# Optimization experiments

Hardware: AMD Instinct MI355X
Metric: run time of the kernel (lower is better)

Reference implementation:

```python
import jax, jax.numpy as jnp
import numpy as np

B, N, DIM = 2, 2048, 1024
NUM_HEADS = 16
EFF = NUM_HEADS // 2          # 8 effective heads
HD = DIM // NUM_HEADS         # 64
LAMBDA_INIT = 0.8
EPS = 1e-5


def setup_inputs() -> dict:
    key = jax.random.key(0)
    ks = jax.random.split(key, 16)
    s = 0.02
    return {
        "x":  jax.random.normal(ks[0], (B, N, DIM), dtype=jnp.float32),
        "Wq": jax.random.normal(ks[1], (DIM, DIM), dtype=jnp.float32) * s,
        "bq": jnp.zeros((DIM,), dtype=jnp.float32),
        "Wk": jax.random.normal(ks[2], (DIM, DIM), dtype=jnp.float32) * s,
        "bk": jnp.zeros((DIM,), dtype=jnp.float32),
        "Wv": jax.random.normal(ks[3], (DIM, DIM), dtype=jnp.float32) * s,
        "bv": jnp.zeros((DIM,), dtype=jnp.float32),
        "Wo": jax.random.normal(ks[4], (DIM, DIM), dtype=jnp.float32) * s,
        "bo": jnp.zeros((DIM,), dtype=jnp.float32),
        "norm_w": jnp.ones((2 * HD,), dtype=jnp.float32),
        "lq1": jax.random.normal(ks[5], (HD,), dtype=jnp.float32) * 0.1,
        "lk1": jax.random.normal(ks[6], (HD,), dtype=jnp.float32) * 0.1,
        "lq2": jax.random.normal(ks[7], (HD,), dtype=jnp.float32) * 0.1,
        "lk2": jax.random.normal(ks[8], (HD,), dtype=jnp.float32) * 0.1,
    }


def reference(x, Wq, bq, Wk, bk, Wv, bv, Wo, bo, norm_w, lq1, lk1, lq2, lk2):
    scale = HD ** -0.5
    # projections (torch Linear: y = x @ W.T + b)
    q = (x @ Wq.T + bq).reshape(B, N, NUM_HEADS, HD).transpose(0, 2, 1, 3) * scale  # [B,2E,N,hd]
    k = (x @ Wk.T + bk).reshape(B, N, NUM_HEADS, HD).transpose(0, 2, 1, 3)          # [B,2E,N,hd]
    v = (x @ Wv.T + bv).reshape(B, N, EFF, 2 * HD).transpose(0, 2, 1, 3)            # [B,E,N,2hd]

    scores = jnp.einsum('bhqd,bhkd->bhqk', q, k)              # [B,2E,N,N]
    probs = jax.nn.softmax(scores, axis=-1)
    probs = probs.reshape(B, EFF, 2, N, N)                    # pair consecutive heads

    lam = jnp.exp(jnp.sum(lq1 * lk1)) - jnp.exp(jnp.sum(lq2 * lk2)) + LAMBDA_INIT
    diff = probs[:, :, 0] - lam * probs[:, :, 1]              # [B,E,N,N]

    out = jnp.einsum('behk,bekd->behd'.replace('e','h').replace('hh','h') if False else 'bhqk,bhkd->bhqd', diff, v)  # [B,E,N,2hd]
    # headwise RMSNorm over last dim (2*hd)
    out = out * jax.lax.rsqrt(jnp.mean(out * out, axis=-1, keepdims=True) + EPS) * norm_w
    out = out * (1.0 - LAMBDA_INIT)

    out = out.transpose(0, 2, 1, 3).reshape(B, N, DIM)
    return out @ Wo.T + bo
```

## Files before the change

### kernel.cpp

```cpp
#include <hip/hip_runtime.h>
#include <hip/hip_bf16.h>

#define B_   2
#define N_   2048
#define DIM_ 1024
#define HD_  64
#define DV_  128

typedef __bf16 bf16;
typedef __bf16 bf16x8 __attribute__((ext_vector_type(8)));
typedef __bf16 bf16x4 __attribute__((ext_vector_type(4)));
typedef float  floatx4 __attribute__((ext_vector_type(4)));

#if __has_builtin(__builtin_amdgcn_exp2f)
#define EXP2(x) __builtin_amdgcn_exp2f(x)
#else
#define EXP2(x) exp2f(x)
#endif

#define QSCALE 0.1803368801111244f

__device__ __forceinline__ void async16(const void* g, void* l) {
  __builtin_amdgcn_global_load_lds(
      (__attribute__((address_space(1))) void*)g,
      (__attribute__((address_space(3))) void*)l, 16, 0, 0);
}

__global__ void convert_kernel(const float* __restrict__ x,
                               const float* __restrict__ wq,
                               const float* __restrict__ wk,
                               const float* __restrict__ wv,
                               const float* __restrict__ wo,
                               bf16* __restrict__ dst) {
  const int NX = B_ * N_ * DIM_;
  const int NW = DIM_ * DIM_;
  int i = (blockIdx.x * 256 + threadIdx.x) * 4;
  const float* src;
  int off;
  if (i < NX) { src = x; off = i; }
  else {
    int j = i - NX;
    int w = j >> 20;
    off = j & (NW - 1);
    src = (w == 0) ? wq : (w == 1) ? wk : (w == 2) ? wv : wo;
  }
  float4 v = *(const float4*)(src + off);
  bf16x4 o = { (bf16)v.x, (bf16)v.y, (bf16)v.z, (bf16)v.w };
  *(bf16x4*)(dst + i) = o;
}

__global__ void lam_kernel(const float* __restrict__ lq1, const float* __restrict__ lk1,
                           const float* __restrict__ lq2, const float* __restrict__ lk2,
                           float* __restrict__ lam_out) {
  int l = threadIdx.x;
  float a = lq1[l] * lk1[l];
  float b = lq2[l] * lk2[l];
  for (int m = 1; m < 64; m <<= 1) {
    a += __shfl_xor(a, m, 64);
    b += __shfl_xor(b, m, 64);
  }
  if (l == 0) *lam_out = __expf(a) - __expf(b) + 0.8f;
}

__global__ __launch_bounds__(256) void proj_kernel(
    const bf16* __restrict__ xb, const bf16* __restrict__ wall,
    const float* __restrict__ bq, const float* __restrict__ bk,
    const float* __restrict__ bv,
    bf16* __restrict__ qo, bf16* __restrict__ ko, bf16* __restrict__ vt) {
  __shared__ __align__(16) bf16 SM[2 * 128 * 64];
  bf16* At = SM;
  bf16* Bt = SM + 128 * 64;
  const int tid = threadIdx.x, lane = tid & 63, w = tid >> 6;
  const int tm = blockIdx.x, tn = blockIdx.y, z = blockIdx.z;
  const int quad = lane >> 4, l15 = lane & 15;
  const int wm = (w >> 1) * 64, wn = (w & 1) * 64;
  const bf16* Ab = xb + (long)tm * 128 * DIM_;
  const bf16* Bb = wall + (long)z * (DIM_ * DIM_) + (long)tn * 128 * DIM_;
  floatx4 zero = {0.f, 0.f, 0.f, 0.f};
  floatx4 acc[4][4];
#pragma unroll
  for (int i = 0; i < 4; ++i)
#pragma unroll
    for (int j = 0; j < 4; ++j) acc[i][j] = zero;

  for (int kb = 0; kb < DIM_ / 64; ++kb) {
    for (int idx = tid; idx < 1024; idx += 256) {
      int row = idx >> 3, ch = idx & 7, g = ch ^ (row & 7);
      async16(Ab + row * DIM_ + kb * 64 + g * 8, (char*)At + (idx - lane) * 16);
      async16(Bb + row * DIM_ + kb * 64 + g * 8, (char*)Bt + (idx - lane) * 16);
    }
    __syncthreads();
#pragma unroll
    for (int ks = 0; ks < 2; ++ks) {
      bf16x8 af[4], bfm[4];
#pragma unroll
      for (int mt = 0; mt < 4; ++mt) {
        int r = wm + mt * 16 + l15;
        af[mt] = *(const bf16x8*)&At[r * 64 + ((ks * 4 + quad) ^ (r & 7)) * 8];
      }
#pragma unroll
      for (int nt = 0; nt < 4; ++nt) {
        int r = wn + nt * 16 + l15;
        bfm[nt] = *(const bf16x8*)&Bt[r * 64 + ((ks * 4 + quad) ^ (r & 7)) * 8];
      }
#pragma unroll
      for (int mt = 0; mt < 4; ++mt)
#pragma unroll
        for (int nt = 0; nt < 4; ++nt)
          acc[mt][nt] = __builtin_amdgcn_mfma_f32_16x16x32_bf16(
              af[mt], bfm[nt], acc[mt][nt], 0, 0, 0);
    }
    __syncthreads();
  }

  if (z != 2) {
#pragma unroll
    for (int mt = 0; mt < 4; ++mt)
#pragma unroll
      for (int nt = 0; nt < 4; ++nt)
#pragma unroll
        for (int r = 0; r < 4; ++r) {
          int grow = tm * 128 + wm + mt * 16 + quad * 4 + r;
          int gcol = tn * 128 + wn + nt * 16 + l15;
          float v = acc[mt][nt][r];
          if (z == 0) {
            qo[(long)grow * DIM_ + gcol] = (bf16)((v + bq[gcol]) * QSCALE);
          } else {
            ko[(long)grow * DIM_ + gcol] = (bf16)(v + bk[gcol]);
          }
        }
  } else {
    bf16* Vl = SM;
#pragma unroll
    for (int nt = 0; nt < 4; ++nt) {
      int d = wn + nt * 16 + l15;
      float bvv = bv[tn * 128 + d];
      int m = (d & 7) * 2;
#pragma unroll
      for (int mt = 0; mt < 4; ++mt) {
        bf16x4 v4 = { (bf16)(acc[mt][nt][0] + bvv), (bf16)(acc[mt][nt][1] + bvv),
                      (bf16)(acc[mt][nt][2] + bvv), (bf16)(acc[mt][nt][3] + bvv) };
        int c = (wm >> 2) + mt * 4 + quad;
        *(bf16x4*)&Vl[d * 128 + (c ^ m) * 4] = v4;
      }
    }
    __syncthreads();
    const int bb = tm >> 4, e = tn;
    const long rowbase = ((long)(bb * 8 + e) * 128) * (long)N_ + (tm & 15) * 128;
#pragma unroll
    for (int p = 0; p < 8; ++p) {
      int d = p * 16 + (tid >> 4), j = tid & 15;
      int cs = (2 * j) ^ ((d & 7) * 2);
      bf16x8 val = *(const bf16x8*)&Vl[d * 128 + cs * 4];
      *(bf16x8*)&vt[rowbase + (long)d * N_ + j * 8] = val;
    }
  }
}

__global__ __launch_bounds__(256, 2) void attn_kernel(
    const bf16* __restrict__ qb, const bf16* __restrict__ kbuf,
    const bf16* __restrict__ vt, const float* __restrict__ lamp,
    const float* __restrict__ norm_w, bf16* __restrict__ ao) {
  __shared__ __align__(16) bf16 Kt[2][2 * 64 * 64];
  __shared__ __align__(16) bf16 Vt[2][128 * 64];
  __shared__ __align__(16) bf16 Pt[4][2][16 * 64];

  const int tid = threadIdx.x, lane = tid & 63, w = tid >> 6;
  const int qt = blockIdx.x, e = blockIdx.y, b = blockIdx.z;
  const int quad = lane >> 4, l15 = lane & 15;
  floatx4 zero = {0.f, 0.f, 0.f, 0.f};

  const int qrow = qt * 64 + w * 16 + l15;
  const bf16* qrp = qb + (long)(b * N_ + qrow) * DIM_ + e * 128;
  bf16x8 qf0[2], qf1[2];
  qf0[0] = *(const bf16x8*)(qrp + quad * 8);
  qf0[1] = *(const bf16x8*)(qrp + 32 + quad * 8);
  qf1[0] = *(const bf16x8*)(qrp + 64 + quad * 8);
  qf1[1] = *(const bf16x8*)(qrp + 96 + quad * 8);

  const bf16* kbase = kbuf + (long)b * N_ * DIM_ + e * 128;
  const bf16* vbase = vt + (long)(b * 8 + e) * DV_ * N_;

  floatx4 acc0[8], acc1[8];
#pragma unroll
  for (int i = 0; i < 8; ++i) { acc0[i] = zero; acc1[i] = zero; }
  float lp0 = 0.f, lp1 = 0.f;

  bf16* Pt0 = Pt[w][0];
  bf16* Pt1 = Pt[w][1];

#define STAGE(ktv, bufv)                                                            \
  {                                                                                 \
    int kt_ = (ktv), buf_ = (bufv);                                                 \
    _Pragma("unroll") for (int t = 0; t < 4; ++t) {                                 \
      int idx = tid + t * 256;                                                      \
      int khl = idx >> 9, row = (idx >> 3) & 63, ch = idx & 7, g = ch ^ (row & 7);  \
      async16(kbase + ((long)(kt_ * 64 + row)) * DIM_ + khl * 64 + g * 8,           \
              (char*)Kt[buf_] + (idx - lane) * 16);                                 \
    }                                                                               \
    _Pragma("unroll") for (int t = 0; t < 4; ++t) {                                 \
      int idx = tid + t * 256;                                                      \
      int row = idx >> 3, ch = idx & 7, g = ch ^ (row & 7);                         \
      async16(vbase + (long)row * N_ + kt_ * 64 + g * 8,                            \
              (char*)Vt[buf_] + (idx - lane) * 16);                                 \
    }                                                                               \
  }

  STAGE(0, 0);

  for (int kt = 0; kt < N_ / 64; ++kt) {
    const int buf = kt & 1;
    __syncthreads();
    if (kt + 1 < N_ / 64) STAGE(kt + 1, buf ^ 1);

    const bf16* Kh0 = Kt[buf];
    const bf16* Kh1 = Kt[buf] + 4096;
    const bf16* Vb = Vt[buf];

    floatx4 s0[4], s1[4];
#pragma unroll
    for (int nt = 0; nt < 4; ++nt) { s0[nt] = zero; s1[nt] = zero; }
#pragma unroll
    for (int ks = 0; ks < 2; ++ks) {
#pragma unroll
      for (int nt = 0; nt < 4; ++nt) {
        int br = nt * 16 + l15;
        int so = ((ks * 4 + quad) ^ (br & 7)) * 8;
        bf16x8 k0 = *(const bf16x8*)&Kh0[br * 64 + so];
        bf16x8 k1 = *(const bf16x8*)&Kh1[br * 64 + so];
        s0[nt] = __builtin_amdgcn_mfma_f32_16x16x32_bf16(k0, qf0[ks], s0[nt], 0, 0, 0);
        s1[nt] = __builtin_amdgcn_mfma_f32_16x16x32_bf16(k1, qf1[ks], s1[nt], 0, 0, 0);
      }
    }

#pragma unroll
    for (int nt = 0; nt < 4; ++nt) {
      float p0 = EXP2(s0[nt][0]), p1 = EXP2(s0[nt][1]);
      float p2 = EXP2(s0[nt][2]), p3 = EXP2(s0[nt][3]);
      lp0 += (p0 + p1) + (p2 + p3);
      bf16x4 v0 = { (bf16)p0, (bf16)p1, (bf16)p2, (bf16)p3 };
      int c = nt * 4 + quad;
      *(bf16x4*)&Pt0[l15 * 64 + (c ^ l15) * 4] = v0;
      float u0 = EXP2(s1[nt][0]), u1 = EXP2(s1[nt][1]);
      float u2 = EXP2(s1[nt][2]), u3 = EXP2(s1[nt][3]);
      lp1 += (u0 + u1) + (u2 + u3);
      bf16x4 v1 = { (bf16)u0, (bf16)u1, (bf16)u2, (bf16)u3 };
      *(bf16x4*)&Pt1[l15 * 64 + (c ^ l15) * 4] = v1;
    }

#pragma unroll
    for (int ks = 0; ks < 2; ++ks) {
      int c0 = 8 * ks + 2 * quad;
      bf16x4 a0lo = *(const bf16x4*)&Pt0[l15 * 64 + ((c0) ^ l15) * 4];
      bf16x4 a0hi = *(const bf16x4*)&Pt0[l15 * 64 + ((c0 + 1) ^ l15) * 4];
      bf16x4 a1lo = *(const bf16x4*)&Pt1[l15 * 64 + ((c0) ^ l15) * 4];
      bf16x4 a1hi = *(const bf16x4*)&Pt1[l15 * 64 + ((c0 + 1) ^ l15) * 4];
      bf16x8 af0 = __builtin_shufflevector(a0lo, a0hi, 0, 1, 2, 3, 4, 5, 6, 7);
      bf16x8 af1 = __builtin_shufflevector(a1lo, a1hi, 0, 1, 2, 3, 4, 5, 6, 7);
#pragma unroll
      for (int dt = 0; dt < 8; ++dt) {
        int br = dt * 16 + l15;
        bf16x8 bfm = *(const bf16x8*)&Vb[br * 64 + ((ks * 4 + quad) ^ (br & 7)) * 8];
        acc0[dt] = __builtin_amdgcn_mfma_f32_16x16x32_bf16(af0, bfm, acc0[dt], 0, 0, 0);
        acc1[dt] = __builtin_amdgcn_mfma_f32_16x16x32_bf16(af1, bfm, acc1[dt], 0, 0, 0);
      }
    }
  }

  lp0 += __shfl_xor(lp0, 16, 64);
  lp0 += __shfl_xor(lp0, 32, 64);
  lp1 += __shfl_xor(lp1, 16, 64);
  lp1 += __shfl_xor(lp1, 32, 64);
  float inv0[4], inv1[4];
#pragma unroll
  for (int r = 0; r < 4; ++r) {
    inv0[r] = 1.0f / __shfl(lp0, quad * 4 + r, 64);
    inv1[r] = 1.0f / __shfl(lp1, quad * 4 + r, 64);
  }

  float lam = *lamp;
  float ss[4] = {0.f, 0.f, 0.f, 0.f};
#pragma unroll
  for (int dt = 0; dt < 8; ++dt)
#pragma unroll
    for (int r = 0; r < 4; ++r) {
      float v = acc0[dt][r] * inv0[r] - lam * (acc1[dt][r] * inv1[r]);
      acc0[dt][r] = v;
      ss[r] += v * v;
    }
  float rms[4];
#pragma unroll
  for (int r = 0; r < 4; ++r) {
    float t = ss[r];
#pragma unroll
    for (int msk = 1; msk < 16; msk <<= 1) t += __shfl_xor(t, msk, 16);
    rms[r] = rsqrtf(t * (1.0f / 128.0f) + 1e-5f);
  }
#pragma unroll
  for (int dt = 0; dt < 8; ++dt) {
    float nwv = norm_w[dt * 16 + l15] * 0.2f;
#pragma unroll
    for (int r = 0; r < 4; ++r) {
      int n = qt * 64 + w * 16 + quad * 4 + r;
      ao[((long)(b * N_ + n)) * DIM_ + e * DV_ + dt * 16 + l15] =
          (bf16)(acc0[dt][r] * rms[r] * nwv);
    }
  }
}

__global__ __launch_bounds__(256) void out_gemm(
    const bf16* __restrict__ ab, const bf16* __restrict__ wo,
    const float* __restrict__ bo, float* __restrict__ out) {
  __shared__ __align__(16) bf16 At[128 * 64];
  __shared__ __align__(16) bf16 Bt[128 * 64];
  const int tid = threadIdx.x, lane = tid & 63, w = tid >> 6;
  const int tm = blockIdx.x, tn = blockIdx.y;
  const int quad = lane >> 4, l15 = lane & 15;
  const int wm = (w >> 1) * 64, wn = (w & 1) * 64;
  const bf16* Ab = ab + (long)tm * 128 * DIM_;
  const bf16* Bb = wo + (long)tn * 128 * DIM_;
  floatx4 zero = {0.f, 0.f, 0.f, 0.f};
  floatx4 acc[4][4];
#pragma unroll
  for (int i = 0; i < 4; ++i)
#pragma unroll
    for (int j = 0; j < 4; ++j) acc[i][j] = zero;

  for (int kb = 0; kb < DIM_ / 64; ++kb) {
    for (int idx = tid; idx < 1024; idx += 256) {
      int row = idx >> 3, ch = idx & 7, g = ch ^ (row & 7);
      async16(Ab + row * DIM_ + kb * 64 + g * 8, (char*)At + (idx - lane) * 16);
      async16(Bb + row * DIM_ + kb * 64 + g * 8, (char*)Bt + (idx - lane) * 16);
    }
    __syncthreads();
#pragma unroll
    for (int ks = 0; ks < 2; ++ks) {
      bf16x8 af[4], bfm[4];
#pragma unroll
      for (int mt = 0; mt < 4; ++mt) {
        int r = wm + mt * 16 + l15;
        af[mt] = *(const bf16x8*)&At[r * 64 + ((ks * 4 + quad) ^ (r & 7)) * 8];
      }
#pragma unroll
      for (int nt = 0; nt < 4; ++nt) {
        int r = wn + nt * 16 + l15;
        bfm[nt] = *(const bf16x8*)&Bt[r * 64 + ((ks * 4 + quad) ^ (r & 7)) * 8];
      }
#pragma unroll
      for (int mt = 0; mt < 4; ++mt)
#pragma unroll
        for (int nt = 0; nt < 4; ++nt)
          acc[mt][nt] = __builtin_amdgcn_mfma_f32_16x16x32_bf16(
              af[mt], bfm[nt], acc[mt][nt], 0, 0, 0);
    }
    __syncthreads();
  }
#pragma unroll
  for (int mt = 0; mt < 4; ++mt)
#pragma unroll
    for (int nt = 0; nt < 4; ++nt)
#pragma unroll
      for (int r = 0; r < 4; ++r) {
        int grow = tm * 128 + wm + mt * 16 + quad * 4 + r;
        int gcol = tn * 128 + wn + nt * 16 + l15;
        out[(long)grow * DIM_ + gcol] = acc[mt][nt][r] + bo[gcol];
      }
}

extern "C" void kernel_launch(void* const* d_in, const int* in_sizes, int n_in,
                              void* d_out, int out_size, void* d_ws, size_t ws_size,
                              hipStream_t stream) {
  const float* x    = (const float*)d_in[0];
  const float* Wq   = (const float*)d_in[1];
  const float* bq   = (const float*)d_in[2];
  const float* Wk   = (const float*)d_in[3];
  const float* bk   = (const float*)d_in[4];
  const float* Wv   = (const float*)d_in[5];
  const float* bv   = (const float*)d_in[6];
  const float* Wo   = (const float*)d_in[7];
  const float* bo   = (const float*)d_in[8];
  const float* nw   = (const float*)d_in[9];
  const float* lq1  = (const float*)d_in[10];
  const float* lk1  = (const float*)d_in[11];
  const float* lq2  = (const float*)d_in[12];
  const float* lk2  = (const float*)d_in[13];

  char* ws = (char*)d_ws;
  float* lam = (float*)ws;
  bf16* xb   = (bf16*)(ws + 256);
  bf16* wqb  = xb + 4194304;
  bf16* qb   = wqb + 4 * 1048576;
  bf16* kbuf = qb + 4194304;
  bf16* vtb  = kbuf + 4194304;
  bf16* ab   = vtb + 4194304;

  convert_kernel<<<8192, 256, 0, stream>>>(x, Wq, Wk, Wv, Wo, xb);
  lam_kernel<<<1, 64, 0, stream>>>(lq1, lk1, lq2, lk2, lam);
  proj_kernel<<<dim3(32, 8, 3), 256, 0, stream>>>(xb, wqb, bq, bk, bv, qb, kbuf, vtb);
  attn_kernel<<<dim3(32, 8, 2), 256, 0, stream>>>(qb, kbuf, vtb, lam, nw, ab);
  out_gemm<<<dim3(32, 8), 256, 0, stream>>>(ab, wqb + 3 * 1048576, bo, (float*)d_out);
}
```

Baseline: 223.3 us.

## Restructure attention to 32x32 MFMA with register-held P and split head-halves across waves

The attention kernel moves from 16x16x32 to 32x32x16 MFMA tiles. Each block now covers 128 queries, and each wave handles one of the two paired heads for 64 queries. The softmax probabilities stay in registers and are rearranged with permlane32_swap, which removes the LDS round trip for P. K and V fragments loaded into registers are reused across two query sub-tiles, and the two heads are combined through an LDS exchange in the epilogue. In exchange the grid halves to 256 blocks at one block per CU with higher register pressure, which risks lower occupancy and weaker latency hiding.

```diff
diff --git a/kernel.cpp b/kernel.cpp
--- a/kernel.cpp
+++ b/kernel.cpp
@@ -11,6 +11,10 @@
 typedef __bf16 bf16x8 __attribute__((ext_vector_type(8)));
 typedef __bf16 bf16x4 __attribute__((ext_vector_type(4)));
 typedef float  floatx4 __attribute__((ext_vector_type(4)));
+typedef float  floatx16 __attribute__((ext_vector_type(16)));
+typedef unsigned int uint;
+typedef uint uint2v __attribute__((ext_vector_type(2)));
+typedef uint uint4v __attribute__((ext_vector_type(4)));
 
 #if __has_builtin(__builtin_amdgcn_exp2f)
 #define EXP2(x) __builtin_amdgcn_exp2f(x)
@@ -24,6 +28,12 @@
   __builtin_amdgcn_global_load_lds(
       (__attribute__((address_space(1))) void*)g,
       (__attribute__((address_space(3))) void*)l, 16, 0, 0);
+}
+
+__device__ __forceinline__ uint packbf(float a, float b) {
+  unsigned short ul = __builtin_bit_cast(unsigned short, (bf16)a);
+  unsigned short uh = __builtin_bit_cast(unsigned short, (bf16)b);
+  return (uint)ul | ((uint)uh << 16);
 }
 
 __global__ void convert_kernel(const float* __restrict__ x,
@@ -157,52 +167,53 @@
   }
 }
 
-__global__ __launch_bounds__(256, 2) void attn_kernel(
+__global__ __launch_bounds__(256, 1) void attn_kernel(
     const bf16* __restrict__ qb, const bf16* __restrict__ kbuf,
     const bf16* __restrict__ vt, const float* __restrict__ lamp,
     const float* __restrict__ norm_w, bf16* __restrict__ ao) {
-  __shared__ __align__(16) bf16 Kt[2][2 * 64 * 64];
-  __shared__ __align__(16) bf16 Vt[2][128 * 64];
-  __shared__ __align__(16) bf16 Pt[4][2][16 * 64];
+  __shared__ __align__(16) char smem[65536];
 
   const int tid = threadIdx.x, lane = tid & 63, w = tid >> 6;
   const int qt = blockIdx.x, e = blockIdx.y, b = blockIdx.z;
-  const int quad = lane >> 4, l15 = lane & 15;
-  floatx4 zero = {0.f, 0.f, 0.f, 0.f};
-
-  const int qrow = qt * 64 + w * 16 + l15;
-  const bf16* qrp = qb + (long)(b * N_ + qrow) * DIM_ + e * 128;
-  bf16x8 qf0[2], qf1[2];
-  qf0[0] = *(const bf16x8*)(qrp + quad * 8);
-  qf0[1] = *(const bf16x8*)(qrp + 32 + quad * 8);
-  qf1[0] = *(const bf16x8*)(qrp + 64 + quad * 8);
-  qf1[1] = *(const bf16x8*)(qrp + 96 + quad * 8);
+  const int hl = w & 1, qh = w >> 1;
+  const int h = lane >> 5, l31 = lane & 31;
+  const int qbase = qt * 128 + qh * 64;
+
+  bf16x8 qf[2][4];
+#pragma unroll
+  for (int qs = 0; qs < 2; ++qs) {
+    const bf16* qrp = qb + (long)(b * N_ + qbase + qs * 32 + l31) * DIM_
+                      + e * 128 + hl * 64 + h * 8;
+#pragma unroll
+    for (int c = 0; c < 4; ++c) qf[qs][c] = *(const bf16x8*)(qrp + c * 16);
+  }
 
   const bf16* kbase = kbuf + (long)b * N_ * DIM_ + e * 128;
   const bf16* vbase = vt + (long)(b * 8 + e) * DV_ * N_;
 
-  floatx4 acc0[8], acc1[8];
-#pragma unroll
-  for (int i = 0; i < 8; ++i) { acc0[i] = zero; acc1[i] = zero; }
-  float lp0 = 0.f, lp1 = 0.f;
-
-  bf16* Pt0 = Pt[w][0];
-  bf16* Pt1 = Pt[w][1];
+  floatx16 acc[2][4];
+#pragma unroll
+  for (int qs = 0; qs < 2; ++qs)
+#pragma unroll
+    for (int dt = 0; dt < 4; ++dt) acc[qs][dt] = floatx16{};
+  float lp[2] = {0.f, 0.f};
 
 #define STAGE(ktv, bufv)                                                            \
   {                                                                                 \
-    int kt_ = (ktv), buf_ = (bufv);                                                 \
+    int kt_ = (ktv);                                                                \
+    char* kdst = smem + (bufv) * 16384;                                             \
+    char* vdst = smem + 32768 + (bufv) * 16384;                                     \
     _Pragma("unroll") for (int t = 0; t < 4; ++t) {                                 \
       int idx = tid + t * 256;                                                      \
       int khl = idx >> 9, row = (idx >> 3) & 63, ch = idx & 7, g = ch ^ (row & 7);  \
       async16(kbase + ((long)(kt_ * 64 + row)) * DIM_ + khl * 64 + g * 8,           \
-              (char*)Kt[buf_] + (idx - lane) * 16);                                 \
+              kdst + (idx - lane) * 16);                                            \
     }                                                                               \
     _Pragma("unroll") for (int t = 0; t < 4; ++t) {                                 \
       int idx = tid + t * 256;                                                      \
       int row = idx >> 3, ch = idx & 7, g = ch ^ (row & 7);                         \
       async16(vbase + (long)row * N_ + kt_ * 64 + g * 8,                            \
-              (char*)Vt[buf_] + (idx - lane) * 16);                                 \
+              vdst + (idx - lane) * 16);                                            \
     }                                                                               \
   }
 
@@ -213,98 +224,118 @@
     __syncthreads();
     if (kt + 1 < N_ / 64) STAGE(kt + 1, buf ^ 1);
 
-    const bf16* Kh0 = Kt[buf];
-    const bf16* Kh1 = Kt[buf] + 4096;
-    const bf16* Vb = Vt[buf];
-
-    floatx4 s0[4], s1[4];
-#pragma unroll
-    for (int nt = 0; nt < 4; ++nt) { s0[nt] = zero; s1[nt] = zero; }
-#pragma unroll
-    for (int ks = 0; ks < 2; ++ks) {
-#pragma unroll
-      for (int nt = 0; nt < 4; ++nt) {
-        int br = nt * 16 + l15;
-        int so = ((ks * 4 + quad) ^ (br & 7)) * 8;
-        bf16x8 k0 = *(const bf16x8*)&Kh0[br * 64 + so];
-        bf16x8 k1 = *(const bf16x8*)&Kh1[br * 64 + so];
-        s0[nt] = __builtin_amdgcn_mfma_f32_16x16x32_bf16(k0, qf0[ks], s0[nt], 0, 0, 0);
-        s1[nt] = __builtin_amdgcn_mfma_f32_16x16x32_bf16(k1, qf1[ks], s1[nt], 0, 0, 0);
-      }
-    }
-
-#pragma unroll
-    for (int nt = 0; nt < 4; ++nt) {
-      float p0 = EXP2(s0[nt][0]), p1 = EXP2(s0[nt][1]);
-      float p2 = EXP2(s0[nt][2]), p3 = EXP2(s0[nt][3]);
-      lp0 += (p0 + p1) + (p2 + p3);
-      bf16x4 v0 = { (bf16)p0, (bf16)p1, (bf16)p2, (bf16)p3 };
-      int c = nt * 4 + quad;
-      *(bf16x4*)&Pt0[l15 * 64 + (c ^ l15) * 4] = v0;
-      float u0 = EXP2(s1[nt][0]), u1 = EXP2(s1[nt][1]);
-      float u2 = EXP2(s1[nt][2]), u3 = EXP2(s1[nt][3]);
-      lp1 += (u0 + u1) + (u2 + u3);
-      bf16x4 v1 = { (bf16)u0, (bf16)u1, (bf16)u2, (bf16)u3 };
-      *(bf16x4*)&Pt1[l15 * 64 + (c ^ l15) * 4] = v1;
-    }
-
-#pragma unroll
-    for (int ks = 0; ks < 2; ++ks) {
-      int c0 = 8 * ks + 2 * quad;
-      bf16x4 a0lo = *(const bf16x4*)&Pt0[l15 * 64 + ((c0) ^ l15) * 4];
-      bf16x4 a0hi = *(const bf16x4*)&Pt0[l15 * 64 + ((c0 + 1) ^ l15) * 4];
-      bf16x4 a1lo = *(const bf16x4*)&Pt1[l15 * 64 + ((c0) ^ l15) * 4];
-      bf16x4 a1hi = *(const bf16x4*)&Pt1[l15 * 64 + ((c0 + 1) ^ l15) * 4];
-      bf16x8 af0 = __builtin_shufflevector(a0lo, a0hi, 0, 1, 2, 3, 4, 5, 6, 7);
-      bf16x8 af1 = __builtin_shufflevector(a1lo, a1hi, 0, 1, 2, 3, 4, 5, 6, 7);
-#pragma unroll
-      for (int dt = 0; dt < 8; ++dt) {
-        int br = dt * 16 + l15;
-        bf16x8 bfm = *(const bf16x8*)&Vb[br * 64 + ((ks * 4 + quad) ^ (br & 7)) * 8];
-        acc0[dt] = __builtin_amdgcn_mfma_f32_16x16x32_bf16(af0, bfm, acc0[dt], 0, 0, 0);
-        acc1[dt] = __builtin_amdgcn_mfma_f32_16x16x32_bf16(af1, bfm, acc1[dt], 0, 0, 0);
-      }
-    }
-  }
-
-  lp0 += __shfl_xor(lp0, 16, 64);
-  lp0 += __shfl_xor(lp0, 32, 64);
-  lp1 += __shfl_xor(lp1, 16, 64);
-  lp1 += __shfl_xor(lp1, 32, 64);
-  float inv0[4], inv1[4];
-#pragma unroll
-  for (int r = 0; r < 4; ++r) {
-    inv0[r] = 1.0f / __shfl(lp0, quad * 4 + r, 64);
-    inv1[r] = 1.0f / __shfl(lp1, quad * 4 + r, 64);
-  }
-
-  float lam = *lamp;
-  float ss[4] = {0.f, 0.f, 0.f, 0.f};
-#pragma unroll
-  for (int dt = 0; dt < 8; ++dt)
-#pragma unroll
-    for (int r = 0; r < 4; ++r) {
-      float v = acc0[dt][r] * inv0[r] - lam * (acc1[dt][r] * inv1[r]);
-      acc0[dt][r] = v;
-      ss[r] += v * v;
-    }
-  float rms[4];
-#pragma unroll
-  for (int r = 0; r < 4; ++r) {
-    float t = ss[r];
-#pragma unroll
-    for (int msk = 1; msk < 16; msk <<= 1) t += __shfl_xor(t, msk, 16);
-    rms[r] = rsqrtf(t * (1.0f / 128.0f) + 1e-5f);
-  }
-#pragma unroll
-  for (int dt = 0; dt < 8; ++dt) {
-    float nwv = norm_w[dt * 16 + l15] * 0.2f;
-#pragma unroll
-    for (int r = 0; r < 4; ++r) {
-      int n = qt * 64 + w * 16 + quad * 4 + r;
-      ao[((long)(b * N_ + n)) * DIM_ + e * DV_ + dt * 16 + l15] =
-          (bf16)(acc0[dt][r] * rms[r] * nwv);
-    }
+    const bf16* Kh = (const bf16*)(smem + buf * 16384) + hl * 4096;
+    const bf16* Vb = (const bf16*)(smem + 32768 + buf * 16384);
+
+    bf16x8 kfrag[2][4], vfrag[4][4];
+#pragma unroll
+    for (int kt2 = 0; kt2 < 2; ++kt2)
+#pragma unroll
+      for (int c = 0; c < 4; ++c) {
+        int row = kt2 * 32 + l31;
+        kfrag[kt2][c] = *(const bf16x8*)&Kh[row * 64 + ((c * 2 + h) ^ (row & 7)) * 8];
+      }
+#pragma unroll
+    for (int dt = 0; dt < 4; ++dt)
+#pragma unroll
+      for (int kc = 0; kc < 4; ++kc) {
+        int row = dt * 32 + l31;
+        vfrag[dt][kc] = *(const bf16x8*)&Vb[row * 64 + ((kc * 2 + h) ^ (row & 7)) * 8];
+      }
+
+#pragma unroll
+    for (int qs = 0; qs < 2; ++qs) {
+      bf16x8 af[2][2];
+#pragma unroll
+      for (int kt2 = 0; kt2 < 2; ++kt2) {
+        floatx16 sv{};
+#pragma unroll
+        for (int c = 0; c < 4; ++c)
+          sv = __builtin_amdgcn_mfma_f32_32x32x16_bf16(kfrag[kt2][c], qf[qs][c], sv, 0, 0, 0);
+        float t[16];
+        float s = 0.f;
+#pragma unroll
+        for (int i = 0; i < 16; ++i) { t[i] = EXP2(sv[i]); s += t[i]; }
+        lp[qs] += s;
+        uint d0 = packbf(t[0], t[1]),   d1 = packbf(t[2], t[3]);
+        uint d2 = packbf(t[4], t[5]),   d3 = packbf(t[6], t[7]);
+        uint d4 = packbf(t[8], t[9]),   d5 = packbf(t[10], t[11]);
+        uint d6 = packbf(t[12], t[13]), d7 = packbf(t[14], t[15]);
+        uint4v f0, f1;
+#if __has_builtin(__builtin_amdgcn_permlane32_swap)
+        uint2v r02 = __builtin_amdgcn_permlane32_swap(d0, d2, false, false);
+        uint2v r13 = __builtin_amdgcn_permlane32_swap(d1, d3, false, false);
+        f0 = uint4v{r02.x, r13.x, r02.y, r13.y};
+        uint2v r46 = __builtin_amdgcn_permlane32_swap(d4, d6, false, false);
+        uint2v r57 = __builtin_amdgcn_permlane32_swap(d5, d7, false, false);
+        f1 = uint4v{r46.x, r57.x, r46.y, r57.y};
+#else
+        uint e0 = __shfl_xor((int)d0, 32, 64), e1 = __shfl_xor((int)d1, 32, 64);
+        uint e2 = __shfl_xor((int)d2, 32, 64), e3 = __shfl_xor((int)d3, 32, 64);
+        uint e4 = __shfl_xor((int)d4, 32, 64), e5 = __shfl_xor((int)d5, 32, 64);
+        uint e6 = __shfl_xor((int)d6, 32, 64), e7 = __shfl_xor((int)d7, 32, 64);
+        f0 = h ? uint4v{e2, e3, d2, d3} : uint4v{d0, d1, e0, e1};
+        f1 = h ? uint4v{e6, e7, d6, d7} : uint4v{d4, d5, e4, e5};
+#endif
+        af[kt2][0] = __builtin_bit_cast(bf16x8, f0);
+        af[kt2][1] = __builtin_bit_cast(bf16x8, f1);
+      }
+#pragma unroll
+      for (int dt = 0; dt < 4; ++dt)
+#pragma unroll
+        for (int kt2 = 0; kt2 < 2; ++kt2)
+#pragma unroll
+          for (int u = 0; u < 2; ++u)
+            acc[qs][dt] = __builtin_amdgcn_mfma_f32_32x32x16_bf16(
+                af[kt2][u], vfrag[dt][kt2 * 2 + u], acc[qs][dt], 0, 0, 0);
+    }
+  }
+
+  lp[0] += __shfl_xor(lp[0], 32, 64);
+  lp[1] += __shfl_xor(lp[1], 32, 64);
+
+  float* Ob = (float*)smem;
+  __syncthreads();
+
+  if (hl == 1) {
+#pragma unroll
+    for (int qs = 0; qs < 2; ++qs)
+#pragma unroll
+      for (int r = 0; r < 16; ++r) {
+        int qloc = (r & 3) + 8 * (r >> 2) + 4 * h;
+        float inv = 1.0f / __shfl(lp[qs], qloc, 64);
+        float* row = &Ob[(qh * 64 + qs * 32 + qloc) * 128 + l31];
+#pragma unroll
+        for (int dt = 0; dt < 4; ++dt) row[dt * 32] = acc[qs][dt][r] * inv;
+      }
+  }
+  __syncthreads();
+  if (hl == 0) {
+    float lam = *lamp;
+    float nw4[4];
+#pragma unroll
+    for (int dt = 0; dt < 4; ++dt) nw4[dt] = norm_w[dt * 32 + l31] * 0.2f;
+#pragma unroll
+    for (int qs = 0; qs < 2; ++qs)
+#pragma unroll
+      for (int r = 0; r < 16; ++r) {
+        int qloc = (r & 3) + 8 * (r >> 2) + 4 * h;
+        float inv = 1.0f / __shfl(lp[qs], qloc, 64);
+        const float* row = &Ob[(qh * 64 + qs * 32 + qloc) * 128 + l31];
+        float v[4], ss = 0.f;
+#pragma unroll
+        for (int dt = 0; dt < 4; ++dt) {
+          v[dt] = acc[qs][dt][r] * inv - lam * row[dt * 32];
+          ss += v[dt] * v[dt];
+        }
+#pragma unroll
+        for (int msk = 1; msk < 32; msk <<= 1) ss += __shfl_xor(ss, msk, 64);
+        float rms = rsqrtf(ss * (1.0f / 128.0f) + 1e-5f);
+        int n = qbase + qs * 32 + qloc;
+        bf16* dst = ao + (long)(b * N_ + n) * DIM_ + e * DV_ + l31;
+#pragma unroll
+        for (int dt = 0; dt < 4; ++dt) dst[dt * 32] = (bf16)(v[dt] * rms * nw4[dt]);
+      }
   }
 }
 
@@ -397,6 +428,6 @@
   convert_kernel<<<8192, 256, 0, stream>>>(x, Wq, Wk, Wv, Wo, xb);
   lam_kernel<<<1, 64, 0, stream>>>(lq1, lk1, lq2, lk2, lam);
   proj_kernel<<<dim3(32, 8, 3), 256, 0, stream>>>(xb, wqb, bq, bk, bv, qb, kbuf, vtb);
-  attn_kernel<<<dim3(32, 8, 2), 256, 0, stream>>>(qb, kbuf, vtb, lam, nw, ab);
+  attn_kernel<<<dim3(16, 8, 2), 256, 0, stream>>>(qb, kbuf, vtb, lam, nw, ab);
   out_gemm<<<dim3(32, 8), 256, 0, stream>>>(ab, wqb + 3 * 1048576, bo, (float*)d_out);
 }
```

New measurement: 222.1 us. No clear change (-0.5%).
